# Performance work log

Hardware: AMD Instinct MI355X
Metric: run time of the kernel (lower is better)

## Reference

```python
import jax, jax.numpy as jnp
import numpy as np

B, N, D = 8, 2048, 512

def setup_inputs() -> dict:
    key = jax.random.key(0)
    ks = jax.random.split(key, 8)
    s = 1.0 / np.sqrt(D)
    return {
        "inputs": jax.random.normal(ks[0], (B, N, D), dtype=jnp.float32),
        "mask": jnp.ones((B, N), dtype=jnp.int32),
        "Wk": jax.random.normal(ks[1], (D, D), dtype=jnp.float32) * s,
        "bk": jax.random.normal(ks[2], (D,), dtype=jnp.float32) * s,
        "Wq": jax.random.normal(ks[3], (D, D), dtype=jnp.float32) * s,
        "bq": jax.random.normal(ks[4], (D,), dtype=jnp.float32) * s,
        "Wv": jax.random.normal(ks[5], (D, D), dtype=jnp.float32) * s,
        "bv": jax.random.normal(ks[6], (D,), dtype=jnp.float32) * s,
    }

def reference(inputs, mask, Wk, bk, Wq, bq, Wv, bv):
    # torch Linear: y = x @ W.T + b
    keys = jnp.einsum('bnd,ed->bne', inputs, Wk) + bk
    queries = jnp.einsum('bnd,ed->bne', inputs, Wq) + bq
    values = jnp.einsum('bnd,ed->bne', inputs, Wv) + bv
    norm = jnp.sqrt(jnp.asarray(D, inputs.dtype))
    scores = jnp.einsum('bqd,bkd->bqk', queries, keys) / norm  # [B,N,N]
    scores = jnp.where(mask[:, None, :] == 0, jnp.asarray(-1e9, scores.dtype), scores)
    attn = jax.nn.softmax(scores, axis=-1)
    return jnp.einsum('bqk,bkd->bqd', attn, values)
```

## Files before the change

### kernel.cpp

```cpp
#include <hip/hip_runtime.h>
#include <hip/hip_bf16.h>


typedef __attribute__((ext_vector_type(8))) short short8;
typedef __attribute__((ext_vector_type(4))) float f32x4;

#define DEV __device__ __forceinline__
#define GLOBAL_AS __attribute__((address_space(1)))
#define LDS_AS __attribute__((address_space(3)))

static DEV ushort f2bs(float f) {
  union { float f; unsigned u; } x; x.f = f;
  unsigned r = (x.u + 0x7fffu + ((x.u >> 16) & 1u)) >> 16;
  return (ushort)r;
}

static DEV f32x4 mfma16(short8 a, short8 b, f32x4 c) {
  return __builtin_amdgcn_mfma_f32_16x16x32_bf16(a, b, c, 0, 0, 0);
}

static DEV void async16(const void* g, void* l) {
  __builtin_amdgcn_global_load_lds((const GLOBAL_AS void*)g, (LDS_AS void*)l, 16, 0, 0);
}

__global__ void convert_w(const float* __restrict__ wq, const float* __restrict__ wk,
                          const float* __restrict__ wv, ushort* __restrict__ wb) {
  int i = blockIdx.x * 256 + threadIdx.x;
  int which = i >> 16;
  int off = (i & 65535) * 4;
  const float* src = (which == 0) ? wq : (which == 1) ? wk : wv;
  float4 v = *(const float4*)(src + off);
  ushort4 o;
  o.x = f2bs(v.x); o.y = f2bs(v.y); o.z = f2bs(v.z); o.w = f2bs(v.w);
  *(ushort4*)(wb + (size_t)which * 262144 + off) = o;
}

__global__ void convert_x(const float* __restrict__ x, ushort* __restrict__ xb) {
  int i = blockIdx.x * 256 + threadIdx.x;
  int off = i * 4;
  float4 v = *(const float4*)(x + off);
  ushort4 o;
  o.x = f2bs(v.x); o.y = f2bs(v.y); o.z = f2bs(v.z); o.w = f2bs(v.w);
  *(ushort4*)(xb + off) = o;
}

__launch_bounds__(256, 2)
__global__ void qkv_gemm(const ushort* __restrict__ Xb, const ushort* __restrict__ Wb,
                         const float* __restrict__ bq, const float* __restrict__ bk,
                         const float* __restrict__ bv,
                         ushort* __restrict__ Qb, ushort* __restrict__ Kb,
                         ushort* __restrict__ Vtb) {
  const int rowblk = blockIdx.x;
  const int colblk = blockIdx.y;
  const int z = colblk >> 2;

  __shared__ ushort As[128 * 64];
  __shared__ ushort Bs[128 * 64];

  const int tid = threadIdx.x;
  const int wave = tid >> 6, lane = tid & 63, quad = lane >> 4, c16 = lane & 15;
  const int wm = wave & 1, wn = wave >> 1;

  f32x4 acc[4][4];
#pragma unroll
  for (int mt = 0; mt < 4; mt++)
#pragma unroll
    for (int nt = 0; nt < 4; nt++) acc[mt][nt] = (f32x4)0.0f;

  const int lr = lane >> 3, lc = lane & 7;
  for (int kb = 0; kb < 512; kb += 64) {
    __syncthreads();
#pragma unroll
    for (int t = 0; t < 8; t++) {
      int idx = wave * 8 + t;
      int rowbase = (idx & 15) * 8;
      int r = rowbase + lr;
      int gc = lc ^ (r & 7);
      if (idx < 16) {
        async16(Xb + (size_t)(rowblk * 128 + r) * 512 + kb + gc * 8, &As[rowbase * 64]);
      } else {
        async16(Wb + (size_t)(colblk * 128 + r) * 512 + kb + gc * 8, &Bs[rowbase * 64]);
      }
    }
    __syncthreads();
#pragma unroll
    for (int kk = 0; kk < 2; kk++) {
      short8 af[4], bfr[4];
#pragma unroll
      for (int t = 0; t < 4; t++) {
        int ra = wm * 64 + t * 16 + c16;
        int rb = wn * 64 + t * 16 + c16;
        af[t]  = *(const short8*)&As[ra * 64 + (((kk * 4 + quad) ^ (ra & 7)) * 8)];
        bfr[t] = *(const short8*)&Bs[rb * 64 + (((kk * 4 + quad) ^ (rb & 7)) * 8)];
      }
#pragma unroll
      for (int mt = 0; mt < 4; mt++)
#pragma unroll
        for (int nt = 0; nt < 4; nt++)
          acc[mt][nt] = mfma16(af[mt], bfr[nt], acc[mt][nt]);
    }
  }

  const float* bias = (z == 0) ? bq : (z == 1) ? bk : bv;
  float bvals[4];
#pragma unroll
  for (int nt = 0; nt < 4; nt++) {
    int eg = colblk * 128 + wn * 64 + nt * 16 + c16;
    bvals[nt] = bias[eg & 511];
  }
  const float sc = (z == 0) ? 0.044194173824159216f : 1.0f;

  const int row0 = rowblk * 128 + wm * 64;
  const int col0 = colblk * 128 + wn * 64;
  if (z < 2) {
    ushort* O = (z == 0) ? Qb : Kb;
#pragma unroll
    for (int mt = 0; mt < 4; mt++)
#pragma unroll
      for (int nt = 0; nt < 4; nt++) {
        int el = (col0 + nt * 16 + c16) & 511;
#pragma unroll
        for (int r = 0; r < 4; r++) {
          int n = row0 + mt * 16 + quad * 4 + r;
          O[(size_t)n * 512 + el] = f2bs((acc[mt][nt][r] + bvals[nt]) * sc);
        }
      }
  } else {
#pragma unroll
    for (int mt = 0; mt < 4; mt++) {
      int grow = row0 + mt * 16 + quad * 4;
      int b = grow >> 11, n0 = grow & 2047;
#pragma unroll
      for (int nt = 0; nt < 4; nt++) {
        int el = (col0 + nt * 16 + c16) & 511;
        ushort4 o;
        o.x = f2bs(acc[mt][nt][0] + bvals[nt]);
        o.y = f2bs(acc[mt][nt][1] + bvals[nt]);
        o.z = f2bs(acc[mt][nt][2] + bvals[nt]);
        o.w = f2bs(acc[mt][nt][3] + bvals[nt]);
        *(ushort4*)(Vtb + ((size_t)b * 512 + el) * 2048 + n0) = o;
      }
    }
  }
}

__launch_bounds__(256, 2)
__global__ void gemm_s(const ushort* __restrict__ Kb, const ushort* __restrict__ Qb,
                       const int* __restrict__ mask, ushort* __restrict__ Pm,
                       float* __restrict__ l) {
  const int b = blockIdx.z;
  const int rowblk = blockIdx.x;
  const int colblk = blockIdx.y;
  const ushort* A = Kb + (size_t)b * 2048 * 512;
  const ushort* Bq = Qb + (size_t)b * 2048 * 512;

  __shared__ ushort As[128 * 64];
  __shared__ ushort Bs[128 * 64];

  const int tid = threadIdx.x;
  const int wave = tid >> 6, lane = tid & 63, quad = lane >> 4, c16 = lane & 15;
  const int wm = wave & 1, wn = wave >> 1;

  f32x4 acc[4][4];
#pragma unroll
  for (int mt = 0; mt < 4; mt++)
#pragma unroll
    for (int nt = 0; nt < 4; nt++) acc[mt][nt] = (f32x4)0.0f;

  const int lr = lane >> 3, lc = lane & 7;
  for (int kb = 0; kb < 512; kb += 64) {
    __syncthreads();
#pragma unroll
    for (int t = 0; t < 8; t++) {
      int idx = wave * 8 + t;
      int rowbase = (idx & 15) * 8;
      int r = rowbase + lr;
      int gc = lc ^ (r & 7);
      if (idx < 16) {
        async16(A  + (size_t)(rowblk * 128 + r) * 512 + kb + gc * 8, &As[rowbase * 64]);
      } else {
        async16(Bq + (size_t)(colblk * 128 + r) * 512 + kb + gc * 8, &Bs[rowbase * 64]);
      }
    }
    __syncthreads();
#pragma unroll
    for (int kk = 0; kk < 2; kk++) {
      short8 af[4], bfr[4];
#pragma unroll
      for (int t = 0; t < 4; t++) {
        int ra = wm * 64 + t * 16 + c16;
        int rb = wn * 64 + t * 16 + c16;
        af[t]  = *(const short8*)&As[ra * 64 + (((kk * 4 + quad) ^ (ra & 7)) * 8)];
        bfr[t] = *(const short8*)&Bs[rb * 64 + (((kk * 4 + quad) ^ (rb & 7)) * 8)];
      }
#pragma unroll
      for (int mt = 0; mt < 4; mt++)
#pragma unroll
        for (int nt = 0; nt < 4; nt++)
          acc[mt][nt] = mfma16(af[mt], bfr[nt], acc[mt][nt]);
    }
  }

  const int row0 = rowblk * 128 + wm * 64;
  const int col0 = colblk * 128 + wn * 64;
  float lpart[4] = {0.0f, 0.0f, 0.0f, 0.0f};
#pragma unroll
  for (int mt = 0; mt < 4; mt++) {
    int key0 = row0 + mt * 16 + quad * 4;
    int4 mv = *(const int4*)&mask[b * 2048 + key0];
    float mf0 = mv.x ? 1.0f : 0.0f, mf1 = mv.y ? 1.0f : 0.0f;
    float mf2 = mv.z ? 1.0f : 0.0f, mf3 = mv.w ? 1.0f : 0.0f;
#pragma unroll
    for (int nt = 0; nt < 4; nt++) {
      int q = col0 + nt * 16 + c16;
      float p0 = __expf(acc[mt][nt][0]) * mf0;
      float p1 = __expf(acc[mt][nt][1]) * mf1;
      float p2 = __expf(acc[mt][nt][2]) * mf2;
      float p3 = __expf(acc[mt][nt][3]) * mf3;
      ushort4 o;
      o.x = f2bs(p0); o.y = f2bs(p1); o.z = f2bs(p2); o.w = f2bs(p3);
      *(ushort4*)(Pm + ((size_t)b * 2048 + q) * 2048 + key0) = o;
      lpart[nt] += p0 + p1 + p2 + p3;
    }
  }
#pragma unroll
  for (int nt = 0; nt < 4; nt++) {
    float v = lpart[nt];
    v += __shfl_xor(v, 16, 64);
    v += __shfl_xor(v, 32, 64);
    if (quad == 0) atomicAdd(&l[b * 2048 + col0 + nt * 16 + c16], v);
  }
}

__launch_bounds__(256, 2)
__global__ void gemm_o(const ushort* __restrict__ Pm, const ushort* __restrict__ Vtb,
                       const float* __restrict__ l, float* __restrict__ out) {
  const int b = blockIdx.z;
  const int rowblk = blockIdx.x;
  const int colblk = blockIdx.y;
  const ushort* A  = Pm  + (size_t)b * 2048 * 2048;
  const ushort* Bv = Vtb + (size_t)b * 512 * 2048;

  __shared__ ushort As[128 * 64];
  __shared__ ushort Bs[128 * 64];

  const int tid = threadIdx.x;
  const int wave = tid >> 6, lane = tid & 63, quad = lane >> 4, c16 = lane & 15;
  const int wm = wave & 1, wn = wave >> 1;

  f32x4 acc[4][4];
#pragma unroll
  for (int mt = 0; mt < 4; mt++)
#pragma unroll
    for (int nt = 0; nt < 4; nt++) acc[mt][nt] = (f32x4)0.0f;

  const int lr = lane >> 3, lc = lane & 7;
  for (int kb = 0; kb < 2048; kb += 64) {
    __syncthreads();
#pragma unroll
    for (int t = 0; t < 8; t++) {
      int idx = wave * 8 + t;
      int rowbase = (idx & 15) * 8;
      int r = rowbase + lr;
      int gc = lc ^ (r & 7);
      if (idx < 16) {
        async16(A  + (size_t)(rowblk * 128 + r) * 2048 + kb + gc * 8, &As[rowbase * 64]);
      } else {
        async16(Bv + (size_t)(colblk * 128 + r) * 2048 + kb + gc * 8, &Bs[rowbase * 64]);
      }
    }
    __syncthreads();
#pragma unroll
    for (int kk = 0; kk < 2; kk++) {
      short8 af[4], bfr[4];
#pragma unroll
      for (int t = 0; t < 4; t++) {
        int ra = wm * 64 + t * 16 + c16;
        int rb = wn * 64 + t * 16 + c16;
        af[t]  = *(const short8*)&As[ra * 64 + (((kk * 4 + quad) ^ (ra & 7)) * 8)];
        bfr[t] = *(const short8*)&Bs[rb * 64 + (((kk * 4 + quad) ^ (rb & 7)) * 8)];
      }
#pragma unroll
      for (int mt = 0; mt < 4; mt++)
#pragma unroll
        for (int nt = 0; nt < 4; nt++)
          acc[mt][nt] = mfma16(af[mt], bfr[nt], acc[mt][nt]);
    }
  }

  const int row0 = rowblk * 128 + wm * 64;
  const int col0 = colblk * 128 + wn * 64;
  float linv[4][4];
#pragma unroll
  for (int mt = 0; mt < 4; mt++)
#pragma unroll
    for (int r = 0; r < 4; r++)
      linv[mt][r] = 1.0f / l[b * 2048 + row0 + mt * 16 + quad * 4 + r];
#pragma unroll
  for (int mt = 0; mt < 4; mt++)
#pragma unroll
    for (int nt = 0; nt < 4; nt++) {
      int col = col0 + nt * 16 + c16;
#pragma unroll
      for (int r = 0; r < 4; r++) {
        int row = row0 + mt * 16 + quad * 4 + r;
        out[((size_t)b * 2048 + row) * 512 + col] = acc[mt][nt][r] * linv[mt][r];
      }
    }
}

extern "C" void kernel_launch(void* const* d_in, const int* in_sizes, int n_in,
                              void* d_out, int out_size, void* d_ws, size_t ws_size,
                              hipStream_t stream) {
  (void)in_sizes; (void)n_in; (void)out_size; (void)ws_size;
  const float* X    = (const float*)d_in[0];
  const int*   mask = (const int*)d_in[1];
  const float* Wk   = (const float*)d_in[2];
  const float* bk   = (const float*)d_in[3];
  const float* Wq   = (const float*)d_in[4];
  const float* bq   = (const float*)d_in[5];
  const float* Wv   = (const float*)d_in[6];
  const float* bv   = (const float*)d_in[7];
  float* out = (float*)d_out;

  ushort* ws  = (ushort*)d_ws;
  ushort* Pm  = ws;
  ushort* Xb  = ws;
  ushort* Wb  = ws + (size_t)33554432;
  ushort* Qb  = Wb + (size_t)786432;
  ushort* Kb  = Qb + (size_t)8388608;
  ushort* Vtb = Kb + (size_t)8388608;
  float*  lde = (float*)(Vtb + (size_t)8388608);

  convert_w<<<768, 256, 0, stream>>>(Wq, Wk, Wv, Wb);
  convert_x<<<8192, 256, 0, stream>>>(X, Xb);
  qkv_gemm<<<dim3(128, 12), 256, 0, stream>>>(Xb, Wb, bq, bk, bv, Qb, Kb, Vtb);
  hipMemsetAsync(lde, 0, 16384 * sizeof(float), stream);
  gemm_s<<<dim3(16, 16, 8), 256, 0, stream>>>(Kb, Qb, mask, Pm, lde);
  gemm_o<<<dim3(16, 4, 8), 256, 0, stream>>>(Pm, Vtb, lde, out);
}
```

Baseline: 233.5 us.

## Merge convert kernels, raise occupancy, remap gemm_s grid, halve gemm_o tile width

Fuses the weight and input bf16 conversion kernels into one launch, which saves a kernel launch. Raises launch bounds from 2 to 4 blocks per CU on all three GEMMs so more waves can hide latency, at the risk of register spills. Flattens the gemm_s grid so consecutive blocks cover different batches. Shrinks the gemm_o N-tile from 128 to 64 to double its block count (512 to 1024) for better CU fill, at the cost of reloading the large P matrix twice as often.

```diff
diff --git a/kernel.cpp b/kernel.cpp
--- a/kernel.cpp
+++ b/kernel.cpp
@@ -23,28 +23,29 @@
   __builtin_amdgcn_global_load_lds((const GLOBAL_AS void*)g, (LDS_AS void*)l, 16, 0, 0);
 }
 
-__global__ void convert_w(const float* __restrict__ wq, const float* __restrict__ wk,
-                          const float* __restrict__ wv, ushort* __restrict__ wb) {
+__global__ void convert_all(const float* __restrict__ wq, const float* __restrict__ wk,
+                            const float* __restrict__ wv, const float* __restrict__ x,
+                            ushort* __restrict__ wb, ushort* __restrict__ xb) {
   int i = blockIdx.x * 256 + threadIdx.x;
-  int which = i >> 16;
-  int off = (i & 65535) * 4;
-  const float* src = (which == 0) ? wq : (which == 1) ? wk : wv;
-  float4 v = *(const float4*)(src + off);
+  const float* src;
+  ushort* dst;
+  if (i < 196608) {
+    int which = i >> 16;
+    int off = (i & 65535) * 4;
+    src = ((which == 0) ? wq : (which == 1) ? wk : wv) + off;
+    dst = wb + (size_t)which * 262144 + off;
+  } else {
+    int off = (i - 196608) * 4;
+    src = x + off;
+    dst = xb + off;
+  }
+  float4 v = *(const float4*)src;
   ushort4 o;
   o.x = f2bs(v.x); o.y = f2bs(v.y); o.z = f2bs(v.z); o.w = f2bs(v.w);
-  *(ushort4*)(wb + (size_t)which * 262144 + off) = o;
-}
-
-__global__ void convert_x(const float* __restrict__ x, ushort* __restrict__ xb) {
-  int i = blockIdx.x * 256 + threadIdx.x;
-  int off = i * 4;
-  float4 v = *(const float4*)(x + off);
-  ushort4 o;
-  o.x = f2bs(v.x); o.y = f2bs(v.y); o.z = f2bs(v.z); o.w = f2bs(v.w);
-  *(ushort4*)(xb + off) = o;
-}
-
-__launch_bounds__(256, 2)
+  *(ushort4*)dst = o;
+}
+
+__launch_bounds__(256, 4)
 __global__ void qkv_gemm(const ushort* __restrict__ Xb, const ushort* __restrict__ Wb,
                          const float* __restrict__ bq, const float* __restrict__ bk,
                          const float* __restrict__ bv,
@@ -144,14 +145,16 @@
   }
 }
 
-__launch_bounds__(256, 2)
+__launch_bounds__(256, 4)
 __global__ void gemm_s(const ushort* __restrict__ Kb, const ushort* __restrict__ Qb,
                        const int* __restrict__ mask, ushort* __restrict__ Pm,
                        float* __restrict__ l) {
-  const int b = blockIdx.z;
-  const int rowblk = blockIdx.x;
-  const int colblk = blockIdx.y;
-  const ushort* A = Kb + (size_t)b * 2048 * 512;
+  const int bid = blockIdx.x;
+  const int b = bid & 7;
+  const int t2 = bid >> 3;
+  const int rowblk = t2 & 15;
+  const int colblk = t2 >> 4;
+  const ushort* A  = Kb + (size_t)b * 2048 * 512;
   const ushort* Bq = Qb + (size_t)b * 2048 * 512;
 
   __shared__ ushort As[128 * 64];
@@ -232,7 +235,7 @@
   }
 }
 
-__launch_bounds__(256, 2)
+__launch_bounds__(256, 4)
 __global__ void gemm_o(const ushort* __restrict__ Pm, const ushort* __restrict__ Vtb,
                        const float* __restrict__ l, float* __restrict__ out) {
   const int b = blockIdx.z;
@@ -242,54 +245,60 @@
   const ushort* Bv = Vtb + (size_t)b * 512 * 2048;
 
   __shared__ ushort As[128 * 64];
-  __shared__ ushort Bs[128 * 64];
+  __shared__ ushort Bs[64 * 64];
 
   const int tid = threadIdx.x;
   const int wave = tid >> 6, lane = tid & 63, quad = lane >> 4, c16 = lane & 15;
   const int wm = wave & 1, wn = wave >> 1;
 
-  f32x4 acc[4][4];
-#pragma unroll
-  for (int mt = 0; mt < 4; mt++)
-#pragma unroll
-    for (int nt = 0; nt < 4; nt++) acc[mt][nt] = (f32x4)0.0f;
+  f32x4 acc[4][2];
+#pragma unroll
+  for (int mt = 0; mt < 4; mt++)
+#pragma unroll
+    for (int nt = 0; nt < 2; nt++) acc[mt][nt] = (f32x4)0.0f;
 
   const int lr = lane >> 3, lc = lane & 7;
   for (int kb = 0; kb < 2048; kb += 64) {
     __syncthreads();
 #pragma unroll
-    for (int t = 0; t < 8; t++) {
-      int idx = wave * 8 + t;
-      int rowbase = (idx & 15) * 8;
-      int r = rowbase + lr;
-      int gc = lc ^ (r & 7);
+    for (int t = 0; t < 6; t++) {
+      int idx = wave * 6 + t;
       if (idx < 16) {
-        async16(A  + (size_t)(rowblk * 128 + r) * 2048 + kb + gc * 8, &As[rowbase * 64]);
+        int rowbase = idx * 8;
+        int r = rowbase + lr;
+        int gc = lc ^ (r & 7);
+        async16(A + (size_t)(rowblk * 128 + r) * 2048 + kb + gc * 8, &As[rowbase * 64]);
       } else {
-        async16(Bv + (size_t)(colblk * 128 + r) * 2048 + kb + gc * 8, &Bs[rowbase * 64]);
+        int rowbase = (idx - 16) * 8;
+        int r = rowbase + lr;
+        int gc = lc ^ (r & 7);
+        async16(Bv + (size_t)(colblk * 64 + r) * 2048 + kb + gc * 8, &Bs[rowbase * 64]);
       }
     }
     __syncthreads();
 #pragma unroll
     for (int kk = 0; kk < 2; kk++) {
-      short8 af[4], bfr[4];
+      short8 af[4], bfr[2];
 #pragma unroll
       for (int t = 0; t < 4; t++) {
         int ra = wm * 64 + t * 16 + c16;
-        int rb = wn * 64 + t * 16 + c16;
-        af[t]  = *(const short8*)&As[ra * 64 + (((kk * 4 + quad) ^ (ra & 7)) * 8)];
+        af[t] = *(const short8*)&As[ra * 64 + (((kk * 4 + quad) ^ (ra & 7)) * 8)];
+      }
+#pragma unroll
+      for (int t = 0; t < 2; t++) {
+        int rb = wn * 32 + t * 16 + c16;
         bfr[t] = *(const short8*)&Bs[rb * 64 + (((kk * 4 + quad) ^ (rb & 7)) * 8)];
       }
 #pragma unroll
       for (int mt = 0; mt < 4; mt++)
 #pragma unroll
-        for (int nt = 0; nt < 4; nt++)
+        for (int nt = 0; nt < 2; nt++)
           acc[mt][nt] = mfma16(af[mt], bfr[nt], acc[mt][nt]);
     }
   }
 
   const int row0 = rowblk * 128 + wm * 64;
-  const int col0 = colblk * 128 + wn * 64;
+  const int col0 = colblk * 64 + wn * 32;
   float linv[4][4];
 #pragma unroll
   for (int mt = 0; mt < 4; mt++)
@@ -299,7 +308,7 @@
 #pragma unroll
   for (int mt = 0; mt < 4; mt++)
 #pragma unroll
-    for (int nt = 0; nt < 4; nt++) {
+    for (int nt = 0; nt < 2; nt++) {
       int col = col0 + nt * 16 + c16;
 #pragma unroll
       for (int r = 0; r < 4; r++) {
@@ -332,10 +341,9 @@
   ushort* Vtb = Kb + (size_t)8388608;
   float*  lde = (float*)(Vtb + (size_t)8388608);
 
-  convert_w<<<768, 256, 0, stream>>>(Wq, Wk, Wv, Wb);
-  convert_x<<<8192, 256, 0, stream>>>(X, Xb);
+  convert_all<<<8960, 256, 0, stream>>>(Wq, Wk, Wv, X, Wb, Xb);
   qkv_gemm<<<dim3(128, 12), 256, 0, stream>>>(Xb, Wb, bq, bk, bv, Qb, Kb, Vtb);
   hipMemsetAsync(lde, 0, 16384 * sizeof(float), stream);
-  gemm_s<<<dim3(16, 16, 8), 256, 0, stream>>>(Kb, Qb, mask, Pm, lde);
-  gemm_o<<<dim3(16, 4, 8), 256, 0, stream>>>(Pm, Vtb, lde, out);
-}
+  gemm_s<<<2048, 256, 0, stream>>>(Kb, Qb, mask, Pm, lde);
+  gemm_o<<<dim3(16, 8, 8), 256, 0, stream>>>(Pm, Vtb, lde, out);
+}
```

Result: slower. 257.5 us (+10.3%).
